# Kernel optimization log

Measured on AMD Instinct MI355X. Metric: run time of the kernel, lower is better.

## Reference

```python
import jax, jax.numpy as jnp
import numpy as np

Q_SCALE = 255.0 / 32.0  # quantization scale used before phi


def setup_inputs() -> dict:
    key = jax.random.key(0)
    ks = jax.random.split(key, 7)
    B, H, W = 8, 384, 384
    PHI, RHO = 32, 64
    x = jax.random.uniform(ks[0], (B, 1, H, W), jnp.float32)
    # Linear weights stored as [in, out]; scaled like torch default init ~1/sqrt(fan_in)
    w1 = jax.random.normal(ks[1], (1, PHI), jnp.float32) * 1.0
    b1 = jax.random.normal(ks[2], (PHI,), jnp.float32) * 0.1
    w2 = jax.random.normal(ks[3], (PHI, PHI), jnp.float32) * (1.0 / np.sqrt(PHI))
    b2 = jax.random.normal(ks[4], (PHI,), jnp.float32) * 0.1
    w3 = jax.random.normal(ks[5], (PHI, RHO), jnp.float32) * (1.0 / np.sqrt(PHI))
    b3 = jax.random.normal(ks[6], (RHO,), jnp.float32) * 0.1
    return {"x": x, "w1": w1, "b1": b1, "w2": w2, "b2": b2, "w3": w3, "b3": b3}


def _extract_3x3(x):
    # x: [B,1,H,W] -> [B,H,W,9] neighborhoods (zero-padded), matching F.unfold(k=3, pad=1)
    B, _, H, W = x.shape
    xp = jnp.pad(x, ((0, 0), (0, 0), (1, 1), (1, 1)))
    return jnp.stack([xp[:, 0, i:i + H, j:j + W] for i in range(3) for j in range(3)], axis=-1)


def reference(x, w1, b1, w2, b2, w3, b3):
    patches = _extract_3x3(x)                       # [B,H,W,9]
    q = jnp.floor(patches * Q_SCALE)                # quantize
    # phi: Linear(1,PHI) + ReLU + Linear(PHI,PHI)
    h = jax.nn.relu(q[..., None] * w1[0] + b1)      # [B,H,W,9,PHI]
    h = jnp.einsum('bhwnc,cd->bhwnd', h, w2) + b2   # [B,H,W,9,PHI]
    agg = h.mean(axis=3)                            # mean over 9 neighbors -> [B,H,W,PHI]
    # rho: Linear(PHI,RHO) + ReLU
    out = jax.nn.relu(jnp.einsum('bhwc,cd->bhwd', agg, w3) + b3)  # [B,H,W,RHO]
    return out.transpose(0, 3, 1, 2)                # [B,RHO,H,W] (fold with k=1 is a reshape)
```

## Files before the change

### kernel.cpp

```cpp
#include <hip/hip_runtime.h>
#include <math.h>

#define Q_SCALE (255.0f / 32.0f)
#define PHI 32
#define RHO 64
#define HH 384
#define WW 384
#define BB 8

__global__ __launch_bounds__(512) void build_table_kernel(
    const float* __restrict__ w1, const float* __restrict__ b1,
    const float* __restrict__ w2, const float* __restrict__ b2,
    const float* __restrict__ w3, float* __restrict__ T) {
    __shared__ float h2[8][PHI];
    const int t = threadIdx.x;
    if (t < 256) {
        const int v = t >> 5, c = t & 31;
        float acc = b2[c];
#pragma unroll
        for (int k = 0; k < PHI; ++k) {
            float h1 = fmaxf((float)v * w1[k] + b1[k], 0.0f);
            acc += h1 * w2[k * PHI + c];
        }
        h2[v][c] = acc;
    }
    __syncthreads();
    {
        const int v = t >> 6, r = t & 63;
        float acc = 0.0f;
#pragma unroll
        for (int c = 0; c < PHI; ++c) acc += h2[v][c] * w3[c * RHO + r];
        T[v * RHO + r] = acc * (1.0f / 9.0f);
    }
}

__global__ __launch_bounds__(WW) void deepset_row_kernel(
    const float* __restrict__ x, const float* __restrict__ Tg,
    const float* __restrict__ b3, float* __restrict__ out) {
    __shared__ unsigned int qe[3][WW + 2];
    __shared__ float Tl[RHO * 8];
    __shared__ float b3l[RHO];

    const int w = threadIdx.x;
    const int bh = blockIdx.x;
    const int h = bh % HH;
    const int b = bh / HH;

    for (int i = w; i < 8 * RHO; i += WW) {
        const int v = i >> 6, r = i & 63;
        Tl[r * 8 + v] = Tg[i];
    }
    if (w < RHO) b3l[w] = b3[w];

    const float* xb = x + (size_t)b * HH * WW;
#pragma unroll
    for (int rr = 0; rr < 3; ++rr) {
        const int hh = h - 1 + rr;
        unsigned int qv = 1u;
        if (hh >= 0 && hh < HH) {
            const float xv = xb[hh * WW + w];
            int q = (int)floorf(xv * Q_SCALE);
            q = q < 0 ? 0 : (q > 7 ? 7 : q);
            qv = 1u << (4 * q);
        }
        qe[rr][w + 1] = qv;
        if (w == 0) { qe[rr][0] = 1u; qe[rr][WW + 1] = 1u; }
    }
    __syncthreads();

    unsigned int cnt = 0;
#pragma unroll
    for (int rr = 0; rr < 3; ++rr)
        cnt += qe[rr][w] + qe[rr][w + 1] + qe[rr][w + 2];

    float c[8];
#pragma unroll
    for (int v = 0; v < 8; ++v) c[v] = (float)((cnt >> (4 * v)) & 15u);

    float* ob = out + ((size_t)b * RHO * HH + h) * WW + w;
    const size_t rstride = (size_t)HH * WW;
#pragma unroll 8
    for (int r = 0; r < RHO; ++r) {
        const float4 t0 = *(const float4*)&Tl[r * 8];
        const float4 t1 = *(const float4*)&Tl[r * 8 + 4];
        float acc = b3l[r];
        acc += c[0] * t0.x + c[1] * t0.y + c[2] * t0.z + c[3] * t0.w;
        acc += c[4] * t1.x + c[5] * t1.y + c[6] * t1.z + c[7] * t1.w;
        ob[r * rstride] = fmaxf(acc, 0.0f);
    }
}

extern "C" void kernel_launch(void* const* d_in, const int* in_sizes, int n_in,
                              void* d_out, int out_size, void* d_ws, size_t ws_size,
                              hipStream_t stream) {
    const float* x  = (const float*)d_in[0];
    const float* w1 = (const float*)d_in[1];
    const float* b1 = (const float*)d_in[2];
    const float* w2 = (const float*)d_in[3];
    const float* b2 = (const float*)d_in[4];
    const float* w3 = (const float*)d_in[5];
    const float* b3 = (const float*)d_in[6];
    float* out = (float*)d_out;
    float* T   = (float*)d_ws;

    build_table_kernel<<<1, 512, 0, stream>>>(w1, b1, w2, b2, w3, T);
    deepset_row_kernel<<<BB * HH, WW, 0, stream>>>(x, T, b3, out);
}
```

Measured before the change: 318.3 us.

## Process four output rows per block with four pixels per thread and float4 stores

The kernel now has each block cover four image rows and each thread compute four adjacent pixels. Per-column vertical sums are shared across the four horizontal windows, and results go out as float4 vector stores. This cuts halo row reloads, table loads per block and the number of store instructions for an output-write-bound kernel. In exchange there are fewer blocks and more registers per thread.

Result: no change. 321.2 us (+0.9%).

```diff
diff --git a/kernel.cpp b/kernel.cpp
--- a/kernel.cpp
+++ b/kernel.cpp
@@ -7,6 +7,9 @@
 #define HH 384
 #define WW 384
 #define BB 8
+#define RPB 4
+#define QPB (WW / 4)
+#define QSTRIDE (WW + 8)
 
 __global__ __launch_bounds__(512) void build_table_kernel(
     const float* __restrict__ w1, const float* __restrict__ b1,
@@ -34,59 +37,94 @@
     }
 }
 
-__global__ __launch_bounds__(WW) void deepset_row_kernel(
+__global__ __launch_bounds__(RPB * QPB) void deepset_quad_kernel(
     const float* __restrict__ x, const float* __restrict__ Tg,
     const float* __restrict__ b3, float* __restrict__ out) {
-    __shared__ unsigned int qe[3][WW + 2];
+    __shared__ unsigned int qe[RPB + 2][QSTRIDE];
     __shared__ float Tl[RHO * 8];
     __shared__ float b3l[RHO];
 
-    const int w = threadIdx.x;
-    const int bh = blockIdx.x;
-    const int h = bh % HH;
-    const int b = bh / HH;
+    const int tid = threadIdx.x;
+    const int blk = blockIdx.x;
+    const int b = blk / (HH / RPB);
+    const int h0 = (blk % (HH / RPB)) * RPB;
 
-    for (int i = w; i < 8 * RHO; i += WW) {
+    for (int i = tid; i < 8 * RHO; i += RPB * QPB) {
         const int v = i >> 6, r = i & 63;
         Tl[r * 8 + v] = Tg[i];
     }
-    if (w < RHO) b3l[w] = b3[w];
+    if (tid < RHO) b3l[tid] = b3[tid];
 
     const float* xb = x + (size_t)b * HH * WW;
+    {
+        const int w = tid;
 #pragma unroll
-    for (int rr = 0; rr < 3; ++rr) {
-        const int hh = h - 1 + rr;
-        unsigned int qv = 1u;
-        if (hh >= 0 && hh < HH) {
-            const float xv = xb[hh * WW + w];
-            int q = (int)floorf(xv * Q_SCALE);
-            q = q < 0 ? 0 : (q > 7 ? 7 : q);
-            qv = 1u << (4 * q);
+        for (int rr = 0; rr < RPB + 2; ++rr) {
+            const int hh = h0 - 1 + rr;
+            unsigned int qv = 1u;
+            if (hh >= 0 && hh < HH) {
+                const float xv = xb[hh * WW + w];
+                int q = (int)floorf(xv * Q_SCALE);
+                q = q < 0 ? 0 : (q > 7 ? 7 : q);
+                qv = 1u << (4 * q);
+            }
+            qe[rr][w + 1] = qv;
         }
-        qe[rr][w + 1] = qv;
-        if (w == 0) { qe[rr][0] = 1u; qe[rr][WW + 1] = 1u; }
+        if (w == 0) {
+#pragma unroll
+            for (int rr = 0; rr < RPB + 2; ++rr) {
+                qe[rr][0] = 1u;
+                qe[rr][WW + 1] = 1u;
+            }
+        }
     }
     __syncthreads();
 
-    unsigned int cnt = 0;
+    const int row = tid / QPB;
+    const int qd = tid % QPB;
+
+    unsigned int cs[6];
 #pragma unroll
-    for (int rr = 0; rr < 3; ++rr)
-        cnt += qe[rr][w] + qe[rr][w + 1] + qe[rr][w + 2];
+    for (int j = 0; j < 6; ++j)
+        cs[j] = qe[row][4 * qd + j] + qe[row + 1][4 * qd + j] + qe[row + 2][4 * qd + j];
 
-    float c[8];
+    const unsigned int cnt0 = cs[0] + cs[1] + cs[2];
+    const unsigned int cnt1 = cs[1] + cs[2] + cs[3];
+    const unsigned int cnt2 = cs[2] + cs[3] + cs[4];
+    const unsigned int cnt3 = cs[3] + cs[4] + cs[5];
+
+    float c0[8], c1[8], c2[8], c3[8];
 #pragma unroll
-    for (int v = 0; v < 8; ++v) c[v] = (float)((cnt >> (4 * v)) & 15u);
+    for (int v = 0; v < 8; ++v) {
+        c0[v] = (float)((cnt0 >> (4 * v)) & 15u);
+        c1[v] = (float)((cnt1 >> (4 * v)) & 15u);
+        c2[v] = (float)((cnt2 >> (4 * v)) & 15u);
+        c3[v] = (float)((cnt3 >> (4 * v)) & 15u);
+    }
 
-    float* ob = out + ((size_t)b * RHO * HH + h) * WW + w;
+    float* op = out + ((size_t)b * RHO * HH + (h0 + row)) * WW + 4 * qd;
     const size_t rstride = (size_t)HH * WW;
 #pragma unroll 8
     for (int r = 0; r < RHO; ++r) {
         const float4 t0 = *(const float4*)&Tl[r * 8];
         const float4 t1 = *(const float4*)&Tl[r * 8 + 4];
-        float acc = b3l[r];
-        acc += c[0] * t0.x + c[1] * t0.y + c[2] * t0.z + c[3] * t0.w;
-        acc += c[4] * t1.x + c[5] * t1.y + c[6] * t1.z + c[7] * t1.w;
-        ob[r * rstride] = fmaxf(acc, 0.0f);
+        const float bb = b3l[r];
+        float a0 = bb, a1 = bb, a2 = bb, a3 = bb;
+        a0 += c0[0] * t0.x + c0[1] * t0.y + c0[2] * t0.z + c0[3] * t0.w;
+        a0 += c0[4] * t1.x + c0[5] * t1.y + c0[6] * t1.z + c0[7] * t1.w;
+        a1 += c1[0] * t0.x + c1[1] * t0.y + c1[2] * t0.z + c1[3] * t0.w;
+        a1 += c1[4] * t1.x + c1[5] * t1.y + c1[6] * t1.z + c1[7] * t1.w;
+        a2 += c2[0] * t0.x + c2[1] * t0.y + c2[2] * t0.z + c2[3] * t0.w;
+        a2 += c2[4] * t1.x + c2[5] * t1.y + c2[6] * t1.z + c2[7] * t1.w;
+        a3 += c3[0] * t0.x + c3[1] * t0.y + c3[2] * t0.z + c3[3] * t0.w;
+        a3 += c3[4] * t1.x + c3[5] * t1.y + c3[6] * t1.z + c3[7] * t1.w;
+        float4 o;
+        o.x = fmaxf(a0, 0.0f);
+        o.y = fmaxf(a1, 0.0f);
+        o.z = fmaxf(a2, 0.0f);
+        o.w = fmaxf(a3, 0.0f);
+        *(float4*)op = o;
+        op += rstride;
     }
 }
 
@@ -104,5 +142,5 @@
     float* T   = (float*)d_ws;
 
     build_table_kernel<<<1, 512, 0, stream>>>(w1, b1, w2, b2, w3, T);
-    deepset_row_kernel<<<BB * HH, WW, 0, stream>>>(x, T, b3, out);
+    deepset_quad_kernel<<<BB * (HH / RPB), RPB * QPB, 0, stream>>>(x, T, b3, out);
 }
```
